# Optimization experiments

Measured on AMD Instinct MI355X. Metric: run time of the kernel, lower is better.

Reference implementation:

```python
import jax, jax.numpy as jnp
import numpy as np

B, S = 32768, 512  # rays, max bright spots (= 2*max_samples)


def setup_inputs() -> dict:
    key = jax.random.key(0)
    k1, k2, k3, k4, k5 = jax.random.split(key, 5)
    V = jax.random.normal(k1, (B, 3), dtype=jnp.float32)
    N = jax.random.normal(k2, (B, 3), dtype=jnp.float32)
    N = N / jnp.linalg.norm(N, axis=-1, keepdims=True)
    spots = jax.random.normal(k3, (S, 3), dtype=jnp.float32)
    spots = spots / jnp.linalg.norm(spots, axis=-1, keepdims=True)
    # prefix masks: num_ele[i] <= num_ray[i] <= S (matches kernel's start_ind-j indexing)
    num_ray = jax.random.randint(k4, (B,), S // 2, S + 1)
    num_ele = jax.random.randint(k5, (B,), 0, S // 2)
    j = jnp.arange(S)
    ray_mask = j[None, :] < num_ray[:, None]
    bright_mask = j[None, :] < num_ele[:, None]
    std = jnp.float32(0.05)  # pix_size
    return {"V": V, "N": N, "spots": spots, "ray_mask": ray_mask,
            "bright_mask": bright_mask, "std": std}


def reference(V, N, spots, ray_mask, bright_mask, std):
    Bn, Sn = bright_mask.shape
    # wp.randf(seed): uniform in [0,1), one per written component -> (B,S,3)
    u = jax.random.uniform(jax.random.key(42), (Bn, Sn, 3), dtype=spots.dtype)
    num_ele = bright_mask.sum(axis=1)            # n per row
    num_ray = ray_mask.sum(axis=1)               # start_ind = num_ray - 1
    j = jnp.arange(Sn)
    active = j[None, :] < num_ele[:, None]       # j in range(n)
    jit = spots[None, :, :] + std * u            # jittered light dirs (B,S,3)
    LdotN = jnp.einsum('bsd,bd->bs', jit, N)
    cond = active & (LdotN > 0.0)                # rejection test
    t = num_ray[:, None] - 1 - j[None, :]        # reversed write index
    t_safe = jnp.where(cond & (t >= 0) & (t < Sn), t, Sn)  # Sn -> dropped
    b_idx = jnp.arange(Bn)[:, None]
    Ls = jnp.zeros((Bn, Sn, 3), spots.dtype).at[b_idx, t_safe].set(jit, mode='drop')
    bmask = jnp.zeros((Bn, Sn), jnp.int32).at[b_idx, t_safe].set(1, mode='drop')
    return Ls, bmask.astype(bool)
```

## Files before the change

### kernel.cpp

```cpp
#include <hip/hip_runtime.h>


#define TF_ROUND(x0, x1, r) { x0 += x1; x1 = ((x1 << (r)) | (x1 >> (32 - (r)))); x1 ^= x0; }

__device__ __forceinline__ unsigned tf2x32_seed42_xor(unsigned x0, unsigned x1) {
  const unsigned k0 = 0u, k1 = 42u;
  const unsigned k2 = 0x1BD11BDAu ^ k0 ^ k1;
  x0 += k0; x1 += k1;
  TF_ROUND(x0,x1,13) TF_ROUND(x0,x1,15) TF_ROUND(x0,x1,26) TF_ROUND(x0,x1,6)
  x0 += k1; x1 += k2 + 1u;
  TF_ROUND(x0,x1,17) TF_ROUND(x0,x1,29) TF_ROUND(x0,x1,16) TF_ROUND(x0,x1,24)
  x0 += k2; x1 += k0 + 2u;
  TF_ROUND(x0,x1,13) TF_ROUND(x0,x1,15) TF_ROUND(x0,x1,26) TF_ROUND(x0,x1,6)
  x0 += k0; x1 += k1 + 3u;
  TF_ROUND(x0,x1,17) TF_ROUND(x0,x1,29) TF_ROUND(x0,x1,16) TF_ROUND(x0,x1,24)
  x0 += k1; x1 += k2 + 4u;
  TF_ROUND(x0,x1,13) TF_ROUND(x0,x1,15) TF_ROUND(x0,x1,26) TF_ROUND(x0,x1,6)
  x0 += k2; x1 += k0 + 5u;
  return x0 ^ x1;
}

typedef float f4v __attribute__((ext_vector_type(4)));

__device__ __forceinline__ int detect_mode(const unsigned char* m) {
  const unsigned char d0 = m[0], d1 = m[1], d4 = m[4];
  return (d0 == 0) ? 3 : ((d1 != 0) ? 0 : ((d4 != 0) ? 1 : 2));
}

__global__ __launch_bounds__(512) void bis_kernel_v4(
    const float* __restrict__ Nrm, const float* __restrict__ spots,
    const unsigned char* __restrict__ rmask, const unsigned char* __restrict__ emask,
    const float* __restrict__ stdp, float* __restrict__ Ls, float* __restrict__ bm,
    int B)
{
  const int tid = threadIdx.x;
  const int rib = tid >> 7;
  const int tr  = tid & 127;
  const int b   = blockIdx.x * 4 + rib;
  const bool valid = (b < B);
  const unsigned base = (unsigned)b * 512u + (unsigned)(tr << 2);

  __shared__ float s_jit[4][512][4];
  __shared__ unsigned s_pack[8];

  const int mode = detect_mode(rmask);

  int rcnt = 0, ecnt = 0;
  if (valid) {
    if (mode == 0) {
      const unsigned rv = *(const unsigned*)(rmask + base);
      const unsigned ev = *(const unsigned*)(emask + base);
      rcnt = __popc(rv & 0x01010101u);
      ecnt = __popc(ev & 0x01010101u);
    } else if (mode == 1) {
      const int4 rv = *(const int4*)((const int*)rmask + base);
      const int4 ev = *(const int4*)((const int*)emask + base);
      rcnt = (rv.x!=0)+(rv.y!=0)+(rv.z!=0)+(rv.w!=0);
      ecnt = (ev.x!=0)+(ev.y!=0)+(ev.z!=0)+(ev.w!=0);
    } else if (mode == 3) {
      const float4 rv = *(const float4*)((const float*)rmask + base);
      const float4 ev = *(const float4*)((const float*)emask + base);
      rcnt = (rv.x!=0.f)+(rv.y!=0.f)+(rv.z!=0.f)+(rv.w!=0.f);
      ecnt = (ev.x!=0.f)+(ev.y!=0.f)+(ev.z!=0.f)+(ev.w!=0.f);
    } else {
      const long long* rp = (const long long*)rmask; const long long* ep = (const long long*)emask;
      #pragma unroll
      for (int c = 0; c < 4; ++c) { rcnt += rp[base+c] != 0; ecnt += ep[base+c] != 0; }
    }
  }
  unsigned pack = (unsigned)rcnt | ((unsigned)ecnt << 16);
  #pragma unroll
  for (int off = 1; off < 64; off <<= 1) pack += __shfl_xor(pack, off, 64);
  if ((tid & 63) == 0) s_pack[tid >> 6] = pack;
  __syncthreads();
  const unsigned rowsum = s_pack[rib * 2] + s_pack[rib * 2 + 1];
  const int num_ray = (int)(rowsum & 0xFFFFu);
  const int num_ele = (int)(rowsum >> 16);

  if (valid && num_ele > 0) {
    const float stdv = stdp[0];
    const float n0 = Nrm[b*3+0], n1 = Nrm[b*3+1], n2 = Nrm[b*3+2];
    for (int j = tr; j < num_ele; j += 128) {
      const unsigned f = ((unsigned)b * 512u + (unsigned)j) * 3u;
      const float u0 = __uint_as_float((tf2x32_seed42_xor(0u, f + 0u) >> 9) | 0x3F800000u) - 1.0f;
      const float u1 = __uint_as_float((tf2x32_seed42_xor(0u, f + 1u) >> 9) | 0x3F800000u) - 1.0f;
      const float u2 = __uint_as_float((tf2x32_seed42_xor(0u, f + 2u) >> 9) | 0x3F800000u) - 1.0f;
      const float j0 = __fadd_rn(spots[j*3+0], __fmul_rn(stdv, u0));
      const float j1 = __fadd_rn(spots[j*3+1], __fmul_rn(stdv, u1));
      const float j2 = __fadd_rn(spots[j*3+2], __fmul_rn(stdv, u2));
      const float d  = __fadd_rn(__fadd_rn(__fmul_rn(j0,n0), __fmul_rn(j1,n1)),
                                 __fmul_rn(j2,n2));
      const bool acc = (d > 0.0f);
      f4v e;
      e.x = acc ? j0 : 0.f; e.y = acc ? j1 : 0.f; e.z = acc ? j2 : 0.f;
      e.w = acc ? 1.f : 0.f;
      *(f4v*)(&s_jit[rib][j][0]) = e;
    }
  }
  __syncthreads();

  if (!valid) return;

  const float* jrow = &s_jit[rib][0][0];
  f4v* lsrow = (f4v*)(Ls + (size_t)b * 1536u);
  #pragma unroll
  for (int i = 0; i < 3; ++i) {
    const int g = i * 128 + tr;
    const unsigned f = (unsigned)(g << 2);
    f4v o;
    #pragma unroll
    for (int k = 0; k < 4; ++k) {
      const unsigned ff = f + k;
      const unsigned s  = (ff * 43691u) >> 17;
      const unsigned comp = ff - 3u * s;
      const int jj = num_ray - 1 - (int)s;
      o[k] = (jj >= 0 && jj < num_ele) ? jrow[(unsigned)jj * 4u + comp] : 0.f;
    }
    lsrow[g] = o;
  }
  {
    f4v mk;
    #pragma unroll
    for (int k = 0; k < 4; ++k) {
      const int s = (tr << 2) + k;
      const int jj = num_ray - 1 - s;
      mk[k] = (jj >= 0 && jj < num_ele) ? jrow[(unsigned)jj * 4u + 3u] : 0.f;
    }
    ((f4v*)(bm + (size_t)b * 512u))[tr] = mk;
  }
}

struct F3 { float x, y, z; };

__global__ __launch_bounds__(512) void bis_kernel_s(
    const float* __restrict__ Nrm, const float* __restrict__ spots,
    const unsigned char* __restrict__ rmask, const unsigned char* __restrict__ emask,
    const float* __restrict__ stdp, float* __restrict__ Ls, float* __restrict__ bm,
    int S)
{
  const long long b = blockIdx.x;
  const int t = threadIdx.x;
  const int mode = detect_mode(rmask);

  const long long e = b * (long long)S + t;
  int rnz, enz;
  if (mode == 0)      { rnz = rmask[e] != 0;                     enz = emask[e] != 0; }
  else if (mode == 1) { rnz = ((const int*)rmask)[e] != 0;       enz = ((const int*)emask)[e] != 0; }
  else if (mode == 2) { rnz = ((const long long*)rmask)[e] != 0; enz = ((const long long*)emask)[e] != 0; }
  else                { rnz = ((const float*)rmask)[e] != 0.0f;  enz = ((const float*)emask)[e] != 0.0f; }

  __shared__ int s_nr[16], s_ne[16];
  const unsigned long long br = __ballot(rnz);
  const unsigned long long be = __ballot(enz);
  const int w = t >> 6;
  if ((t & 63) == 0) { s_nr[w] = __popcll(br); s_ne[w] = __popcll(be); }
  __syncthreads();
  const int nw = blockDim.x >> 6;
  int num_ray = 0, num_ele = 0;
  for (int i = 0; i < nw; ++i) { num_ray += s_nr[i]; num_ele += s_ne[i]; }

  const int j = num_ray - 1 - t;
  float o0 = 0.f, o1 = 0.f, o2 = 0.f, m = 0.f;
  if (j >= 0 && j < num_ele) {
    const float stdv = stdp[0];
    const float n0 = Nrm[b*3+0], n1 = Nrm[b*3+1], n2 = Nrm[b*3+2];
    const unsigned f = (unsigned)((b * (long long)S + j) * 3LL);
    const float u0 = __uint_as_float((tf2x32_seed42_xor(0u, f + 0u) >> 9) | 0x3F800000u) - 1.0f;
    const float u1 = __uint_as_float((tf2x32_seed42_xor(0u, f + 1u) >> 9) | 0x3F800000u) - 1.0f;
    const float u2 = __uint_as_float((tf2x32_seed42_xor(0u, f + 2u) >> 9) | 0x3F800000u) - 1.0f;
    const float j0 = __fadd_rn(spots[j*3+0], __fmul_rn(stdv, u0));
    const float j1 = __fadd_rn(spots[j*3+1], __fmul_rn(stdv, u1));
    const float j2 = __fadd_rn(spots[j*3+2], __fmul_rn(stdv, u2));
    const float d  = __fadd_rn(__fadd_rn(__fmul_rn(j0,n0), __fmul_rn(j1,n1)), __fmul_rn(j2,n2));
    if (d > 0.0f) { o0 = j0; o1 = j1; o2 = j2; m = 1.0f; }
  }

  const long long oidx = b * (long long)S + t;
  F3 v; v.x = o0; v.y = o1; v.z = o2;
  reinterpret_cast<F3*>(Ls)[oidx] = v;
  bm[oidx] = m;
}

extern "C" void kernel_launch(void* const* d_in, const int* in_sizes, int n_in,
                              void* d_out, int out_size, void* d_ws, size_t ws_size,
                              hipStream_t stream) {
  const float* Nrm = (const float*)d_in[1];
  const float* spots = (const float*)d_in[2];
  const unsigned char* rmask = (const unsigned char*)d_in[3];
  const unsigned char* emask = (const unsigned char*)d_in[4];
  const float* stdp = (const float*)d_in[5];

  const int B = in_sizes[0] / 3;
  const int S = in_sizes[2] / 3;

  float* out = (float*)d_out;
  float* Ls = out;
  float* bm = out + (long long)B * S * 3;

  if (S == 512) {
    dim3 grid((unsigned)((B + 3) / 4)), block(512);
    hipLaunchKernelGGL(bis_kernel_v4, grid, block, 0, stream,
                       Nrm, spots, rmask, emask, stdp, Ls, bm, B);
  } else {
    dim3 grid((unsigned)B), block((unsigned)S);
    hipLaunchKernelGGL(bis_kernel_s, grid, block, 0, stream,
                       Nrm, spots, rmask, emask, stdp, Ls, bm, S);
  }
}
```

Baseline: 91.60 us.

## Map one ray per 64-thread wavefront block and skip out-of-range output segments

Replaces the 4-rays-per-512-thread block with a single-wavefront block per ray, so the row reduction needs only a wave shuffle and no shared-memory pass or extra barrier. Shared memory per block drops to 4 KB, which allows many more resident blocks. Output quads whose index range falls outside [num_ray-num_ele, num_ray) skip the LDS gathers and write zeros directly. In exchange each lane does twice the load and RNG work, and the grid becomes 32768 small blocks.

```diff
diff --git a/kernel.cpp b/kernel.cpp
--- a/kernel.cpp
+++ b/kernel.cpp
@@ -27,60 +27,51 @@
   return (d0 == 0) ? 3 : ((d1 != 0) ? 0 : ((d4 != 0) ? 1 : 2));
 }
 
-__global__ __launch_bounds__(512) void bis_kernel_v4(
+__global__ __launch_bounds__(64, 8) void bis_row(
     const float* __restrict__ Nrm, const float* __restrict__ spots,
     const unsigned char* __restrict__ rmask, const unsigned char* __restrict__ emask,
-    const float* __restrict__ stdp, float* __restrict__ Ls, float* __restrict__ bm,
-    int B)
+    const float* __restrict__ stdp, float* __restrict__ Ls, float* __restrict__ bm)
 {
-  const int tid = threadIdx.x;
-  const int rib = tid >> 7;
-  const int tr  = tid & 127;
-  const int b   = blockIdx.x * 4 + rib;
-  const bool valid = (b < B);
-  const unsigned base = (unsigned)b * 512u + (unsigned)(tr << 2);
-
-  __shared__ float s_jit[4][512][4];
-  __shared__ unsigned s_pack[8];
+  const int b = blockIdx.x;
+  const int l = threadIdx.x;
+  __shared__ f4v s_jit[256];
 
   const int mode = detect_mode(rmask);
+  const unsigned base = (unsigned)b * 512u + (unsigned)(l << 3);
 
   int rcnt = 0, ecnt = 0;
-  if (valid) {
-    if (mode == 0) {
-      const unsigned rv = *(const unsigned*)(rmask + base);
-      const unsigned ev = *(const unsigned*)(emask + base);
-      rcnt = __popc(rv & 0x01010101u);
-      ecnt = __popc(ev & 0x01010101u);
-    } else if (mode == 1) {
-      const int4 rv = *(const int4*)((const int*)rmask + base);
-      const int4 ev = *(const int4*)((const int*)emask + base);
-      rcnt = (rv.x!=0)+(rv.y!=0)+(rv.z!=0)+(rv.w!=0);
-      ecnt = (ev.x!=0)+(ev.y!=0)+(ev.z!=0)+(ev.w!=0);
-    } else if (mode == 3) {
-      const float4 rv = *(const float4*)((const float*)rmask + base);
-      const float4 ev = *(const float4*)((const float*)emask + base);
-      rcnt = (rv.x!=0.f)+(rv.y!=0.f)+(rv.z!=0.f)+(rv.w!=0.f);
-      ecnt = (ev.x!=0.f)+(ev.y!=0.f)+(ev.z!=0.f)+(ev.w!=0.f);
-    } else {
-      const long long* rp = (const long long*)rmask; const long long* ep = (const long long*)emask;
-      #pragma unroll
-      for (int c = 0; c < 4; ++c) { rcnt += rp[base+c] != 0; ecnt += ep[base+c] != 0; }
-    }
+  if (mode == 0) {
+    const uint2 rv = *(const uint2*)(rmask + base);
+    const uint2 ev = *(const uint2*)(emask + base);
+    rcnt = __popc(rv.x & 0x01010101u) + __popc(rv.y & 0x01010101u);
+    ecnt = __popc(ev.x & 0x01010101u) + __popc(ev.y & 0x01010101u);
+  } else if (mode == 1) {
+    const int* rp = (const int*)rmask + base; const int* ep = (const int*)emask + base;
+    const int4 r0 = *(const int4*)rp, r1 = *(const int4*)(rp + 4);
+    const int4 e0 = *(const int4*)ep, e1 = *(const int4*)(ep + 4);
+    rcnt = (r0.x!=0)+(r0.y!=0)+(r0.z!=0)+(r0.w!=0)+(r1.x!=0)+(r1.y!=0)+(r1.z!=0)+(r1.w!=0);
+    ecnt = (e0.x!=0)+(e0.y!=0)+(e0.z!=0)+(e0.w!=0)+(e1.x!=0)+(e1.y!=0)+(e1.z!=0)+(e1.w!=0);
+  } else if (mode == 3) {
+    const float* rp = (const float*)rmask + base; const float* ep = (const float*)emask + base;
+    const float4 r0 = *(const float4*)rp, r1 = *(const float4*)(rp + 4);
+    const float4 e0 = *(const float4*)ep, e1 = *(const float4*)(ep + 4);
+    rcnt = (r0.x!=0.f)+(r0.y!=0.f)+(r0.z!=0.f)+(r0.w!=0.f)+(r1.x!=0.f)+(r1.y!=0.f)+(r1.z!=0.f)+(r1.w!=0.f);
+    ecnt = (e0.x!=0.f)+(e0.y!=0.f)+(e0.z!=0.f)+(e0.w!=0.f)+(e1.x!=0.f)+(e1.y!=0.f)+(e1.z!=0.f)+(e1.w!=0.f);
+  } else {
+    const long long* rp = (const long long*)rmask; const long long* ep = (const long long*)emask;
+    #pragma unroll
+    for (int c = 0; c < 8; ++c) { rcnt += rp[base+c] != 0; ecnt += ep[base+c] != 0; }
   }
   unsigned pack = (unsigned)rcnt | ((unsigned)ecnt << 16);
   #pragma unroll
   for (int off = 1; off < 64; off <<= 1) pack += __shfl_xor(pack, off, 64);
-  if ((tid & 63) == 0) s_pack[tid >> 6] = pack;
-  __syncthreads();
-  const unsigned rowsum = s_pack[rib * 2] + s_pack[rib * 2 + 1];
-  const int num_ray = (int)(rowsum & 0xFFFFu);
-  const int num_ele = (int)(rowsum >> 16);
-
-  if (valid && num_ele > 0) {
+  const int num_ray = (int)(pack & 0xFFFFu);
+  const int num_ele = (int)(pack >> 16);
+
+  if (num_ele > 0) {
     const float stdv = stdp[0];
     const float n0 = Nrm[b*3+0], n1 = Nrm[b*3+1], n2 = Nrm[b*3+2];
-    for (int j = tr; j < num_ele; j += 128) {
+    for (int j = l; j < num_ele; j += 64) {
       const unsigned f = ((unsigned)b * 512u + (unsigned)j) * 3u;
       const float u0 = __uint_as_float((tf2x32_seed42_xor(0u, f + 0u) >> 9) | 0x3F800000u) - 1.0f;
       const float u1 = __uint_as_float((tf2x32_seed42_xor(0u, f + 1u) >> 9) | 0x3F800000u) - 1.0f;
@@ -91,42 +82,52 @@
       const float d  = __fadd_rn(__fadd_rn(__fmul_rn(j0,n0), __fmul_rn(j1,n1)),
                                  __fmul_rn(j2,n2));
       const bool acc = (d > 0.0f);
-      f4v e;
-      e.x = acc ? j0 : 0.f; e.y = acc ? j1 : 0.f; e.z = acc ? j2 : 0.f;
+      f4v e; e.x = acc ? j0 : 0.f; e.y = acc ? j1 : 0.f; e.z = acc ? j2 : 0.f;
       e.w = acc ? 1.f : 0.f;
-      *(f4v*)(&s_jit[rib][j][0]) = e;
+      s_jit[j] = e;
     }
   }
   __syncthreads();
 
-  if (!valid) return;
-
-  const float* jrow = &s_jit[rib][0][0];
+  const int lo = num_ray - num_ele;
+  const int hi = num_ray;
+  const float* jrow = (const float*)s_jit;
+
   f4v* lsrow = (f4v*)(Ls + (size_t)b * 1536u);
   #pragma unroll
-  for (int i = 0; i < 3; ++i) {
-    const int g = i * 128 + tr;
-    const unsigned f = (unsigned)(g << 2);
-    f4v o;
-    #pragma unroll
-    for (int k = 0; k < 4; ++k) {
-      const unsigned ff = f + k;
-      const unsigned s  = (ff * 43691u) >> 17;
-      const unsigned comp = ff - 3u * s;
-      const int jj = num_ray - 1 - (int)s;
-      o[k] = (jj >= 0 && jj < num_ele) ? jrow[(unsigned)jj * 4u + comp] : 0.f;
+  for (int i = 0; i < 6; ++i) {
+    const int g = i * 64 + l;
+    const unsigned ff0 = (unsigned)(g << 2);
+    const int s0 = (int)((ff0 * 43691u) >> 17);
+    const int s1 = (int)(((ff0 + 3u) * 43691u) >> 17);
+    f4v o = {0.f, 0.f, 0.f, 0.f};
+    if (s1 >= lo && s0 < hi) {
+      #pragma unroll
+      for (int k = 0; k < 4; ++k) {
+        const unsigned ff = ff0 + (unsigned)k;
+        const unsigned s  = (ff * 43691u) >> 17;
+        const unsigned comp = ff - 3u * s;
+        const int jj = num_ray - 1 - (int)s;
+        if (jj >= 0 && jj < num_ele) o[k] = jrow[(unsigned)jj * 4u + comp];
+      }
     }
     lsrow[g] = o;
   }
-  {
-    f4v mk;
-    #pragma unroll
-    for (int k = 0; k < 4; ++k) {
-      const int s = (tr << 2) + k;
-      const int jj = num_ray - 1 - s;
-      mk[k] = (jj >= 0 && jj < num_ele) ? jrow[(unsigned)jj * 4u + 3u] : 0.f;
+
+  f4v* bmrow = (f4v*)(bm + (size_t)b * 512u);
+  #pragma unroll
+  for (int i = 0; i < 2; ++i) {
+    const int g = i * 64 + l;
+    const int sb = g << 2;
+    f4v o = {0.f, 0.f, 0.f, 0.f};
+    if (sb + 3 >= lo && sb < hi) {
+      #pragma unroll
+      for (int k = 0; k < 4; ++k) {
+        const int jj = num_ray - 1 - (sb + k);
+        if (jj >= 0 && jj < num_ele) o[k] = jrow[(unsigned)jj * 4u + 3u];
+      }
     }
-    ((f4v*)(bm + (size_t)b * 512u))[tr] = mk;
+    bmrow[g] = o;
   }
 }
 
@@ -198,9 +199,9 @@
   float* bm = out + (long long)B * S * 3;
 
   if (S == 512) {
-    dim3 grid((unsigned)((B + 3) / 4)), block(512);
-    hipLaunchKernelGGL(bis_kernel_v4, grid, block, 0, stream,
-                       Nrm, spots, rmask, emask, stdp, Ls, bm, B);
+    dim3 grid((unsigned)B), block(64);
+    hipLaunchKernelGGL(bis_row, grid, block, 0, stream,
+                       Nrm, spots, rmask, emask, stdp, Ls, bm);
   } else {
     dim3 grid((unsigned)B), block((unsigned)S);
     hipLaunchKernelGGL(bis_kernel_s, grid, block, 0, stream,
```

Result: faster. 82.88 us (-9.5%).
